# Performance work log

Hardware: AMD Instinct MI355X
Metric: run time of the kernel (lower is better)

The kernel has to match this reference:

```python
import jax, jax.numpy as jnp
import numpy as np

N = 50000        # num nodes (hyperedge ids also live in [0, N), matching old PyG quirk)
E = 1600000      # num incidence pairs
F_IN = 512       # input features
HEADS = 8
OUT1 = 8         # hconv1 out_channels per head
HID = HEADS * OUT1  # 64
NCLS = 7
NEG_SLOPE = 0.2


def setup_inputs() -> dict:
    key = jax.random.key(0)
    ks = jax.random.split(key, 8)
    x = jax.random.normal(ks[0], (N, F_IN), dtype=jnp.float32)
    edge_index = jax.random.randint(ks[1], (2, E), 0, N, dtype=jnp.int32)
    hyperedge_weight = jax.random.uniform(ks[2], (N,), dtype=jnp.float32) + 0.1
    W1 = jax.random.normal(ks[3], (F_IN, HEADS * OUT1), dtype=jnp.float32) * (1.0 / np.sqrt(F_IN))
    att1 = jax.random.normal(ks[4], (1, HEADS, 2 * OUT1), dtype=jnp.float32) * 0.1
    b1 = jnp.zeros((HEADS * OUT1,), dtype=jnp.float32)
    W2 = jax.random.normal(ks[5], (HID, NCLS), dtype=jnp.float32) * (1.0 / np.sqrt(HID))
    b2 = jnp.zeros((NCLS,), dtype=jnp.float32)
    return {"x": x, "edge_index": edge_index, "hyperedge_weight": hyperedge_weight,
            "W1": W1, "att1": att1, "b1": b1, "W2": W2, "b2": b2}


def _segment_softmax(a, seg, n):
    # numerically-stable softmax over groups defined by seg (per column / head)
    amax = jax.ops.segment_max(a, seg, num_segments=n)
    amax = jnp.where(jnp.isfinite(amax), amax, 0.0)
    ex = jnp.exp(a - amax[seg])
    den = jax.ops.segment_sum(ex, seg, num_segments=n)
    return ex / (den[seg] + 1e-16)


def _hconv(x, edge_index, hw, W, bias, heads, out_ch, att=None):
    """Old-PyG HypergraphConv forward (dropout disabled / eval mode)."""
    row, col = edge_index[0], edge_index[1]   # row: node ids, col: hyperedge ids
    n = x.shape[0]
    ones = jnp.ones(row.shape[0], dtype=x.dtype)
    xh = (x @ W).reshape(n, heads, out_ch)    # [N, H, C]

    if att is not None:
        # split att to avoid materializing cat([x_i, x_j]) per edge
        s_i = (xh * att[..., :out_ch]).sum(-1)   # [N, H]
        s_j = (xh * att[..., out_ch:]).sum(-1)   # [N, H]
        a = jax.nn.leaky_relu(s_i[row] + s_j[col], NEG_SLOPE)  # [E, H]
        alpha = _segment_softmax(a, row, n)      # grouped by source node
    else:
        alpha = None

    # node degree norm D (weighted by hyperedge weight)
    D = jax.ops.segment_sum(hw[col], row, num_segments=n)
    Dinv = jnp.where(D > 0, 1.0 / D, 0.0)
    # hyperedge degree norm B, scaled by hyperedge weight
    Bdeg = jax.ops.segment_sum(ones, col, num_segments=n)
    Binv = jnp.where(Bdeg > 0, 1.0 / Bdeg, 0.0) * hw

    # propagate 1: nodes -> hyperedges, norm = B[target]
    msg1 = xh[row] * Binv[col][:, None, None]          # [E, H, C]
    if alpha is not None:
        msg1 = msg1 * alpha[:, :, None]
    out_e = jax.ops.segment_sum(msg1, col, num_segments=n)  # [N, H, C]

    # propagate 2: hyperedges -> nodes, norm = D[target]
    msg2 = out_e[col] * Dinv[row][:, None, None]       # [E, H, C]
    if alpha is not None:
        msg2 = msg2 * alpha[:, :, None]
    out = jax.ops.segment_sum(msg2, row, num_segments=n)    # [N, H, C]

    return out.reshape(n, heads * out_ch) + bias   # concat=True


def reference(x, edge_index, hyperedge_weight, W1, att1, b1, W2, b2):
    # eval mode: F.dropout(p=0.6) is identity
    h = jax.nn.elu(_hconv(x, edge_index, hyperedge_weight, W1, b1, HEADS, OUT1, att1))
    out = _hconv(h, edge_index, hyperedge_weight, W2, b2, 1, NCLS, None)
    return jax.nn.log_softmax(out, axis=1)
```

## Files before the change

kernel.cpp:

```cpp
#include <hip/hip_runtime.h>
#include <hip/hip_bf16.h>
#include <cmath>

#define NN    50000
#define EE    1600000
#define FIN   512
#define NHEAD 8
#define OUT1  8
#define HID   64
#define NCLS  7

#define NB    391
#define EPB   4096
#define LOG2E 1.4426950408889634f

#define OFF_XH     0
#define OFF_SJ     3200000
#define OFF_SIRD   3600000
#define OFF_DINV   4400000
#define OFF_BINV   4450000
#define OFF_ACCE   4500000
#define OFF_H      7700000
#define OFF_XH2    10900000
#define OFF_ACCE2  11300000
#define OFF_RPTR   11700000
#define OFF_CPTR   11760000
#define OFF_BHR    11820000
#define OFF_BHC    11821000
#define OFF_BSR    11822000
#define OFF_BSC    11823000
#define OFF_BCR    11824000
#define OFF_BCC    11825000
#define OFF_CSRRC  11830000
#define OFF_CSRCR  13430000

#define LRELU(a) ((a) > 0.f ? (a) : 0.2f * (a))

__device__ __forceinline__ float fexp2(float x) {
#if __has_builtin(__builtin_amdgcn_exp2f)
  return __builtin_amdgcn_exp2f(x);
#else
  return exp2f(x);
#endif
}

__global__ __launch_bounds__(512) void zero_small(int* __restrict__ bh_r,
                                                  int* __restrict__ bh_c) {
  int t = threadIdx.x;
  if (t <= NB) { bh_r[t] = 0; bh_c[t] = 0; }
}

__global__ __launch_bounds__(256) void bucket_hist(const int* __restrict__ ei,
                                                   int* __restrict__ bh_r,
                                                   int* __restrict__ bh_c) {
  __shared__ int hr[NB], hc[NB];
  int t = threadIdx.x;
  for (int i = t; i < NB; i += 256) { hr[i] = 0; hc[i] = 0; }
  __syncthreads();
  for (int i = blockIdx.x * 256 + t; i < EE; i += gridDim.x * 256) {
    atomicAdd(hr + (ei[i] >> 7), 1);
    atomicAdd(hc + (ei[EE + i] >> 7), 1);
  }
  __syncthreads();
  for (int i = t; i < NB; i += 256) {
    if (hr[i]) atomicAdd(bh_r + i, hr[i]);
    if (hc[i]) atomicAdd(bh_c + i, hc[i]);
  }
}

__global__ __launch_bounds__(512) void bucket_scan(const int* __restrict__ bh_r,
                                                   const int* __restrict__ bh_c,
                                                   int* __restrict__ bs_r,
                                                   int* __restrict__ bs_c,
                                                   int* __restrict__ bc_r,
                                                   int* __restrict__ bc_c) {
  __shared__ int lds[512];
  int t = threadIdx.x;
  for (int side = 0; side < 2; ++side) {
    const int* bh = side ? bh_c : bh_r;
    int* bs = side ? bs_c : bs_r;
    int* bc = side ? bc_c : bc_r;
    int v = (t < NB) ? bh[t] : 0;
    lds[t] = v;
    __syncthreads();
    for (int off = 1; off < 512; off <<= 1) {
      int u = (t >= off) ? lds[t - off] : 0;
      __syncthreads();
      lds[t] += u;
      __syncthreads();
    }
    int excl = lds[t] - v;
    if (t <= NB) bs[t] = excl;
    if (t < NB) bc[t] = excl;
    __syncthreads();
  }
}

__global__ __launch_bounds__(256) void phaseA(const int* __restrict__ ei,
                                              int* __restrict__ bc_r,
                                              int* __restrict__ bc_c,
                                              int* __restrict__ tmp_r,
                                              int* __restrict__ tmp_c) {
  __shared__ int er[EPB];
  __shared__ int ec[EPB];
  __shared__ int hr[NB], hc[NB];
  const int e0 = blockIdx.x * EPB;
  const int cntE = min(EPB, EE - e0);
  const int t = threadIdx.x;
  for (int i = t; i < cntE; i += 256) { er[i] = ei[e0 + i]; ec[i] = ei[EE + e0 + i]; }
  for (int i = t; i < NB; i += 256) { hr[i] = 0; hc[i] = 0; }
  __syncthreads();
  for (int i = t; i < cntE; i += 256) {
    atomicAdd(hr + (er[i] >> 7), 1);
    atomicAdd(hc + (ec[i] >> 7), 1);
  }
  __syncthreads();
  for (int i = t; i < NB; i += 256) {
    int n = hr[i];
    hr[i] = n ? atomicAdd(bc_r + i, n) : 0;
    n = hc[i];
    hc[i] = n ? atomicAdd(bc_c + i, n) : 0;
  }
  __syncthreads();
  for (int i = t; i < cntE; i += 256) {
    int r = er[i], c = ec[i];
    int pr = atomicAdd(hr + (r >> 7), 1);
    tmp_r[pr] = ((r & 127) << 16) | c;
    int pc = atomicAdd(hc + (c >> 7), 1);
    tmp_c[pc] = ((c & 127) << 16) | r;
  }
}

__global__ __launch_bounds__(256) void phaseB(const int* __restrict__ tmp_r,
                                              const int* __restrict__ tmp_c,
                                              const int* __restrict__ bs_r,
                                              const int* __restrict__ bs_c,
                                              const float* __restrict__ hw,
                                              int* __restrict__ rptr,
                                              int* __restrict__ cptr,
                                              int* __restrict__ csr_row_c,
                                              int* __restrict__ csr_col_r,
                                              float* __restrict__ Binv) {
  const int side = blockIdx.x >= NB ? 1 : 0;
  const int b = blockIdx.x - side * NB;
  const int* tmp = side ? tmp_c : tmp_r;
  const int* bs = side ? bs_c : bs_r;
  int* ptr = side ? cptr : rptr;
  int* csr = side ? csr_col_r : csr_row_c;

  const int base = bs[b];
  const int M = bs[b + 1] - base;
  __shared__ int cnt[128], pre[128], cur[128];
  const int t = threadIdx.x;
  if (t < 128) cnt[t] = 0;
  __syncthreads();
  for (int i = t; i < M; i += 256) atomicAdd(cnt + (tmp[base + i] >> 16), 1);
  __syncthreads();
  if (t < 128) pre[t] = cnt[t];
  __syncthreads();
  for (int off = 1; off < 128; off <<= 1) {
    int u = (t >= off && t < 128) ? pre[t - off] : 0;
    __syncthreads();
    if (t < 128) pre[t] += u;
    __syncthreads();
  }
  const int node0 = b << 7;
  if (t < 128) {
    int excl = pre[t] - cnt[t];
    int g = node0 + t;
    if (g <= NN) ptr[g] = base + excl;
    cur[t] = base + excl;
    if (side && g < NN) Binv[g] = cnt[t] > 0 ? hw[g] / (float)cnt[t] : 0.f;
  }
  __syncthreads();
  for (int i = t; i < M; i += 256) {
    int e = tmp[base + i];
    int pos = atomicAdd(cur + (e >> 16), 1);
    csr[pos] = e & 0xFFFF;
  }
}

__global__ __launch_bounds__(256) void gemm1_kernel(const float* __restrict__ x,
                                                    const float* __restrict__ W1,
                                                    float* __restrict__ xh) {
  __shared__ float lx[32][68];
  __shared__ float lw[32][68];
  const int t = threadIdx.x;
  const int row0 = blockIdx.x * 64;
  const int ty = t >> 4, tx = t & 15;
  const int r0 = ty * 4, c0 = tx * 4;
  float acc[4][4] = {};

  for (int kb = 0; kb < FIN; kb += 32) {
    {
      int lr = t >> 2;
      int lk = (t & 3) * 8;
      int grow = row0 + lr;
      float4 a0, a1;
      if (grow < NN) {
        const float4* p = reinterpret_cast<const float4*>(x + (size_t)grow * FIN + kb + lk);
        a0 = p[0]; a1 = p[1];
      } else {
        a0 = make_float4(0.f, 0.f, 0.f, 0.f); a1 = a0;
      }
      lx[lk + 0][lr] = a0.x; lx[lk + 1][lr] = a0.y;
      lx[lk + 2][lr] = a0.z; lx[lk + 3][lr] = a0.w;
      lx[lk + 4][lr] = a1.x; lx[lk + 5][lr] = a1.y;
      lx[lk + 6][lr] = a1.z; lx[lk + 7][lr] = a1.w;
    }
    {
      int wk = t >> 3;
      int wc = (t & 7) * 8;
      const float4* q = reinterpret_cast<const float4*>(W1 + (size_t)(kb + wk) * HID + wc);
      float4 b0 = q[0], b1v = q[1];
      *reinterpret_cast<float4*>(&lw[wk][wc]) = b0;
      *reinterpret_cast<float4*>(&lw[wk][wc + 4]) = b1v;
    }
    __syncthreads();
#pragma unroll
    for (int kk = 0; kk < 32; ++kk) {
      const float4 af = *reinterpret_cast<const float4*>(&lx[kk][r0]);
      const float4 bf = *reinterpret_cast<const float4*>(&lw[kk][c0]);
      const float a4[4] = {af.x, af.y, af.z, af.w};
      const float b4[4] = {bf.x, bf.y, bf.z, bf.w};
#pragma unroll
      for (int i = 0; i < 4; ++i)
#pragma unroll
        for (int j = 0; j < 4; ++j)
          acc[i][j] = fmaf(a4[i], b4[j], acc[i][j]);
    }
    __syncthreads();
  }
#pragma unroll
  for (int i = 0; i < 4; ++i) {
    int gr = row0 + r0 + i;
    if (gr < NN) {
      float4 v = make_float4(acc[i][0], acc[i][1], acc[i][2], acc[i][3]);
      *reinterpret_cast<float4*>(xh + (size_t)gr * HID + c0) = v;
    }
  }
}

__global__ __launch_bounds__(256) void attscore_kernel(const float* __restrict__ xh,
                                                       const float* __restrict__ att1,
                                                       float2* __restrict__ sird,
                                                       float* __restrict__ s_j) {
  int t = blockIdx.x * 256 + threadIdx.x;
  if (t >= NN * NHEAD) return;
  int n = t >> 3, hh = t & 7;
  const float* xp = xh + (size_t)n * HID + hh * OUT1;
  float si = 0.f, sj = 0.f;
#pragma unroll
  for (int c = 0; c < OUT1; ++c) {
    float v = xp[c];
    si = fmaf(v, att1[hh * 16 + c], si);
    sj = fmaf(v, att1[hh * 16 + 8 + c], sj);
  }
  sird[t] = make_float2(si * LOG2E, 0.f);
  s_j[t] = sj * LOG2E;
}

__global__ __launch_bounds__(256) void den_csr(const int* __restrict__ rptr,
                                               const int* __restrict__ csr_row_c,
                                               const float* __restrict__ s_j,
                                               const float* __restrict__ hw,
                                               float2* __restrict__ sird,
                                               float* __restrict__ dinv) {
  int wid = (blockIdx.x * 256 + threadIdx.x) >> 6;
  int lane = threadIdx.x & 63;
  if (wid >= NN) return;
  int r = wid;
  int hh = lane & 7;
  int eslot = lane >> 3;
  float si = sird[r * 8 + hh].x;
  int beg = rptr[r], end = rptr[r + 1];
  float aexp = 0.f, ad = 0.f;
  int i = beg + eslot;
  for (; i + 8 < end; i += 16) {
    int c0 = csr_row_c[i], c1 = csr_row_c[i + 8];
    float sj0 = s_j[c0 * 8 + hh], sj1 = s_j[c1 * 8 + hh];
    float h0 = hw[c0], h1 = hw[c1];
    float a0 = LRELU(si + sj0), a1 = LRELU(si + sj1);
    aexp += fexp2(a0) + fexp2(a1);
    ad += h0 + h1;
  }
  if (i < end) {
    int c = csr_row_c[i];
    float a = LRELU(si + s_j[c * 8 + hh]);
    aexp += fexp2(a);
    ad += hw[c];
  }
  aexp += __shfl_xor(aexp, 8);
  aexp += __shfl_xor(aexp, 16);
  aexp += __shfl_xor(aexp, 32);
  ad += __shfl_xor(ad, 8);
  ad += __shfl_xor(ad, 16);
  ad += __shfl_xor(ad, 32);
  if (eslot == 0) {
    reinterpret_cast<float*>(sird)[(r * 8 + hh) * 2 + 1] = 1.0f / (aexp + 1e-16f);
    if (hh == 0) dinv[r] = ad > 0.f ? 1.0f / ad : 0.f;
  }
}

__global__ __launch_bounds__(256) void prop1_csr(const int* __restrict__ cptr,
                                                 const int* __restrict__ csr_col_r,
                                                 const float* __restrict__ xh,
                                                 const float2* __restrict__ sird,
                                                 const float* __restrict__ s_j,
                                                 const float* __restrict__ Binv,
                                                 float* __restrict__ acc_e) {
  int wid = (blockIdx.x * 256 + threadIdx.x) >> 6;
  int lane = threadIdx.x & 63;
  if (wid >= NN) return;
  const int c = wid;
  const int hh = lane >> 3;
  const int j = lane & 7;
  const int abase = lane & 56;
  float sj = s_j[c * 8 + hh];
  int beg = cptr[c], end = cptr[c + 1];
  float acc = 0.f;
  int i = beg;
  for (; i + 8 <= end; i += 8) {
    int rj = csr_col_r[i + j];
    float2 q = sird[rj * 8 + hh];
    float a = LRELU(q.x + sj);
    float aexp = fexp2(a) * q.y;
#pragma unroll
    for (int j2 = 0; j2 < 8; ++j2) {
      int r = __shfl(rj, j2);
      float al = __shfl(aexp, abase + j2);
      acc = fmaf(xh[(r << 6) + lane], al, acc);
    }
  }
  for (; i < end; ++i) {
    int r = csr_col_r[i];
    float2 q = sird[r * 8 + hh];
    float a = LRELU(q.x + sj);
    acc = fmaf(xh[(r << 6) + lane], fexp2(a) * q.y, acc);
  }
  acc_e[(c << 6) + lane] = acc * Binv[c];
}

__global__ __launch_bounds__(256) void prop2_csr(const int* __restrict__ rptr,
                                                 const int* __restrict__ csr_row_c,
                                                 const float* __restrict__ acc_e,
                                                 const float2* __restrict__ sird,
                                                 const float* __restrict__ s_j,
                                                 const float* __restrict__ dinv,
                                                 const float* __restrict__ b1,
                                                 float* __restrict__ h) {
  int wid = (blockIdx.x * 256 + threadIdx.x) >> 6;
  int lane = threadIdx.x & 63;
  if (wid >= NN) return;
  const int r = wid;
  const int hh = lane >> 3;
  const int j = lane & 7;
  const int abase = lane & 56;
  float2 sr = sird[r * 8 + hh];
  const float si = sr.x, rd = sr.y;
  int beg = rptr[r], end = rptr[r + 1];
  float acc = 0.f;
  int i = beg;
  for (; i + 8 <= end; i += 8) {
    int cj = csr_row_c[i + j];
    float sjv = s_j[cj * 8 + hh];
    float aexp = fexp2(LRELU(si + sjv));
#pragma unroll
    for (int j2 = 0; j2 < 8; ++j2) {
      int cc = __shfl(cj, j2);
      float al = __shfl(aexp, abase + j2);
      acc = fmaf(acc_e[(cc << 6) + lane], al, acc);
    }
  }
  for (; i < end; ++i) {
    int cc = csr_row_c[i];
    float aexp = fexp2(LRELU(si + s_j[cc * 8 + hh]));
    acc = fmaf(acc_e[(cc << 6) + lane], aexp, acc);
  }
  acc *= rd;
  float v = fmaf(acc, dinv[r], b1[lane]);
  h[(r << 6) + lane] = v > 0.f ? v : expm1f(v);
}

__global__ __launch_bounds__(256) void gemm2_kernel(const float* __restrict__ h,
                                                    const float* __restrict__ W2,
                                                    float* __restrict__ xh2) {
  int t = blockIdx.x * 256 + threadIdx.x;
  if (t >= NN * 8) return;
  int n = t >> 3, k = t & 7;
  if (k == 7) { xh2[t] = 0.f; return; }
  const float* hp = h + (size_t)n * HID;
  float acc = 0.f;
#pragma unroll
  for (int c = 0; c < HID; ++c) acc = fmaf(hp[c], W2[c * NCLS + k], acc);
  xh2[t] = acc;
}

__global__ __launch_bounds__(256) void prop3_csr(const int* __restrict__ cptr,
                                                 const int* __restrict__ csr_col_r,
                                                 const float* __restrict__ xh2,
                                                 const float* __restrict__ Binv,
                                                 float* __restrict__ acc_e2) {
  int t = blockIdx.x * 256 + threadIdx.x;
  int g = t >> 3, k = t & 7;
  if (g >= NN) return;
  int beg = cptr[g], end = cptr[g + 1];
  float acc = 0.f;
  int i = beg;
  for (; i + 3 < end; i += 4) {
    int r0 = csr_col_r[i], r1 = csr_col_r[i + 1];
    int r2 = csr_col_r[i + 2], r3 = csr_col_r[i + 3];
    float v0 = xh2[r0 * 8 + k], v1 = xh2[r1 * 8 + k];
    float v2 = xh2[r2 * 8 + k], v3 = xh2[r3 * 8 + k];
    acc += (v0 + v1) + (v2 + v3);
  }
  for (; i < end; ++i) acc += xh2[csr_col_r[i] * 8 + k];
  acc_e2[g * 8 + k] = acc * Binv[g];
}

__global__ __launch_bounds__(256) void prop4_csr(const int* __restrict__ rptr,
                                                 const int* __restrict__ csr_row_c,
                                                 const float* __restrict__ acc_e2,
                                                 const float* __restrict__ dinv,
                                                 const float* __restrict__ b2,
                                                 float* __restrict__ out) {
  int t = blockIdx.x * 256 + threadIdx.x;
  int r = t >> 3, k = t & 7;
  if (r >= NN) return;
  int beg = rptr[r], end = rptr[r + 1];
  float acc = 0.f;
  int i = beg;
  for (; i + 3 < end; i += 4) {
    int c0 = csr_row_c[i], c1 = csr_row_c[i + 1];
    int c2 = csr_row_c[i + 2], c3 = csr_row_c[i + 3];
    float v0 = acc_e2[c0 * 8 + k], v1 = acc_e2[c1 * 8 + k];
    float v2 = acc_e2[c2 * 8 + k], v3 = acc_e2[c3 * 8 + k];
    acc += (v0 + v1) + (v2 + v3);
  }
  for (; i < end; ++i) acc += acc_e2[csr_row_c[i] * 8 + k];
  float v = (k < NCLS) ? fmaf(acc, dinv[r], b2[k]) : -INFINITY;
  float m = v;
  m = fmaxf(m, __shfl_xor(m, 1, 8));
  m = fmaxf(m, __shfl_xor(m, 2, 8));
  m = fmaxf(m, __shfl_xor(m, 4, 8));
  float ex = (k < NCLS) ? expf(v - m) : 0.f;
  float s = ex;
  s += __shfl_xor(s, 1, 8);
  s += __shfl_xor(s, 2, 8);
  s += __shfl_xor(s, 4, 8);
  float lse = m + logf(s);
  if (k < NCLS) out[(size_t)r * NCLS + k] = v - lse;
}

extern "C" void kernel_launch(void* const* d_in, const int* in_sizes, int n_in,
                              void* d_out, int out_size, void* d_ws, size_t ws_size,
                              hipStream_t stream) {
  const float* x    = (const float*)d_in[0];
  const int*   ei   = (const int*)d_in[1];
  const float* hw   = (const float*)d_in[2];
  const float* W1   = (const float*)d_in[3];
  const float* att1 = (const float*)d_in[4];
  const float* b1   = (const float*)d_in[5];
  const float* W2   = (const float*)d_in[6];
  const float* b2   = (const float*)d_in[7];
  float* out = (float*)d_out;
  float* ws  = (float*)d_ws;

  float* xh     = ws + OFF_XH;
  float* s_j    = ws + OFF_SJ;
  float2* sird  = (float2*)(ws + OFF_SIRD);
  float* dinv   = ws + OFF_DINV;
  float* Binv   = ws + OFF_BINV;
  float* acc_e  = ws + OFF_ACCE;
  float* hbuf   = ws + OFF_H;
  float* xh2    = ws + OFF_XH2;
  float* acc_e2 = ws + OFF_ACCE2;
  int* rptr = (int*)(ws + OFF_RPTR);
  int* cptr = (int*)(ws + OFF_CPTR);
  int* bh_r = (int*)(ws + OFF_BHR);
  int* bh_c = (int*)(ws + OFF_BHC);
  int* bs_r = (int*)(ws + OFF_BSR);
  int* bs_c = (int*)(ws + OFF_BSC);
  int* bc_r = (int*)(ws + OFF_BCR);
  int* bc_c = (int*)(ws + OFF_BCC);
  int* csr_row_c = (int*)(ws + OFF_CSRRC);
  int* csr_col_r = (int*)(ws + OFF_CSRCR);
  int* tmp_r = (int*)(ws + OFF_XH);
  int* tmp_c = (int*)(ws + OFF_ACCE);

  zero_small<<<1, 512, 0, stream>>>(bh_r, bh_c);
  bucket_hist<<<256, 256, 0, stream>>>(ei, bh_r, bh_c);
  bucket_scan<<<1, 512, 0, stream>>>(bh_r, bh_c, bs_r, bs_c, bc_r, bc_c);
  phaseA<<<(EE + EPB - 1) / EPB, 256, 0, stream>>>(ei, bc_r, bc_c, tmp_r, tmp_c);
  phaseB<<<2 * NB, 256, 0, stream>>>(tmp_r, tmp_c, bs_r, bs_c, hw,
                                     rptr, cptr, csr_row_c, csr_col_r, Binv);

  gemm1_kernel<<<(NN + 63) / 64, 256, 0, stream>>>(x, W1, xh);
  attscore_kernel<<<(NN * NHEAD + 255) / 256, 256, 0, stream>>>(xh, att1, sird, s_j);
  den_csr<<<(NN * 64 + 255) / 256, 256, 0, stream>>>(rptr, csr_row_c, s_j, hw, sird, dinv);
  prop1_csr<<<(NN * 64 + 255) / 256, 256, 0, stream>>>(cptr, csr_col_r, xh, sird, s_j, Binv, acc_e);
  prop2_csr<<<(NN * 64 + 255) / 256, 256, 0, stream>>>(rptr, csr_row_c, acc_e, sird, s_j,
                                                       dinv, b1, hbuf);

  gemm2_kernel<<<(NN * 8 + 255) / 256, 256, 0, stream>>>(hbuf, W2, xh2);
  prop3_csr<<<(NN * 8 + 255) / 256, 256, 0, stream>>>(cptr, csr_col_r, xh2, Binv, acc_e2);
  prop4_csr<<<(NN * 8 + 255) / 256, 256, 0, stream>>>(rptr, csr_row_c, acc_e2, dinv, b2, out);
}
```

Before: 354.0 us.

## Double-buffer LDS tiles in gemm1 with register prefetch of next K-slice

```diff
diff --git a/kernel.cpp b/kernel.cpp
--- a/kernel.cpp
+++ b/kernel.cpp
@@ -183,44 +183,66 @@
 __global__ __launch_bounds__(256) void gemm1_kernel(const float* __restrict__ x,
                                                     const float* __restrict__ W1,
                                                     float* __restrict__ xh) {
-  __shared__ float lx[32][68];
-  __shared__ float lw[32][68];
+  __shared__ float lx[2][32][68];
+  __shared__ float lw[2][32][68];
   const int t = threadIdx.x;
   const int row0 = blockIdx.x * 64;
   const int ty = t >> 4, tx = t & 15;
   const int r0 = ty * 4, c0 = tx * 4;
+  const bool isX = t < 128;
+  const int srow = t & 63;
+  const int sk = (t >> 6) * 16;
+  const int wu = t - 128;
+  const int wk = wu >> 2;
+  const int wc = (wu & 3) * 16;
+
+  float4 p0, p1, p2, p3;
+
+#define G1_PREFETCH(kb)                                                      \
+  {                                                                          \
+    if (isX) {                                                               \
+      int grow = row0 + srow;                                                \
+      if (grow < NN) {                                                       \
+        const float4* p = reinterpret_cast<const float4*>(                   \
+            x + (size_t)grow * FIN + (kb) + sk);                             \
+        p0 = p[0]; p1 = p[1]; p2 = p[2]; p3 = p[3];                          \
+      } else {                                                               \
+        p0 = make_float4(0.f, 0.f, 0.f, 0.f); p1 = p0; p2 = p0; p3 = p0;     \
+      }                                                                      \
+    } else {                                                                 \
+      const float4* q = reinterpret_cast<const float4*>(                     \
+          W1 + (size_t)((kb) + wk) * HID + wc);                              \
+      p0 = q[0]; p1 = q[1]; p2 = q[2]; p3 = q[3];                            \
+    }                                                                        \
+  }
+
+#define G1_COMMIT(buf)                                                       \
+  {                                                                          \
+    if (isX) {                                                               \
+      float v[16] = {p0.x, p0.y, p0.z, p0.w, p1.x, p1.y, p1.z, p1.w,         \
+                     p2.x, p2.y, p2.z, p2.w, p3.x, p3.y, p3.z, p3.w};        \
+      _Pragma("unroll")                                                      \
+      for (int i = 0; i < 16; ++i) lx[buf][sk + i][srow] = v[i];             \
+    } else {                                                                 \
+      *reinterpret_cast<float4*>(&lw[buf][wk][wc + 0])  = p0;                \
+      *reinterpret_cast<float4*>(&lw[buf][wk][wc + 4])  = p1;                \
+      *reinterpret_cast<float4*>(&lw[buf][wk][wc + 8])  = p2;                \
+      *reinterpret_cast<float4*>(&lw[buf][wk][wc + 12]) = p3;                \
+    }                                                                        \
+  }
+
   float acc[4][4] = {};
-
-  for (int kb = 0; kb < FIN; kb += 32) {
-    {
-      int lr = t >> 2;
-      int lk = (t & 3) * 8;
-      int grow = row0 + lr;
-      float4 a0, a1;
-      if (grow < NN) {
-        const float4* p = reinterpret_cast<const float4*>(x + (size_t)grow * FIN + kb + lk);
-        a0 = p[0]; a1 = p[1];
-      } else {
-        a0 = make_float4(0.f, 0.f, 0.f, 0.f); a1 = a0;
-      }
-      lx[lk + 0][lr] = a0.x; lx[lk + 1][lr] = a0.y;
-      lx[lk + 2][lr] = a0.z; lx[lk + 3][lr] = a0.w;
-      lx[lk + 4][lr] = a1.x; lx[lk + 5][lr] = a1.y;
-      lx[lk + 6][lr] = a1.z; lx[lk + 7][lr] = a1.w;
-    }
-    {
-      int wk = t >> 3;
-      int wc = (t & 7) * 8;
-      const float4* q = reinterpret_cast<const float4*>(W1 + (size_t)(kb + wk) * HID + wc);
-      float4 b0 = q[0], b1v = q[1];
-      *reinterpret_cast<float4*>(&lw[wk][wc]) = b0;
-      *reinterpret_cast<float4*>(&lw[wk][wc + 4]) = b1v;
-    }
-    __syncthreads();
+  G1_PREFETCH(0);
+  G1_COMMIT(0);
+  __syncthreads();
+
+  for (int tt = 0; tt < FIN / 32; ++tt) {
+    const int cur = tt & 1;
+    if (tt < FIN / 32 - 1) G1_PREFETCH((tt + 1) * 32);
 #pragma unroll
     for (int kk = 0; kk < 32; ++kk) {
-      const float4 af = *reinterpret_cast<const float4*>(&lx[kk][r0]);
-      const float4 bf = *reinterpret_cast<const float4*>(&lw[kk][c0]);
+      const float4 af = *reinterpret_cast<const float4*>(&lx[cur][kk][r0]);
+      const float4 bf = *reinterpret_cast<const float4*>(&lw[cur][kk][c0]);
       const float a4[4] = {af.x, af.y, af.z, af.w};
       const float b4[4] = {bf.x, bf.y, bf.z, bf.w};
 #pragma unroll
@@ -229,8 +251,12 @@
         for (int j = 0; j < 4; ++j)
           acc[i][j] = fmaf(a4[i], b4[j], acc[i][j]);
     }
+    if (tt < FIN / 32 - 1) G1_COMMIT(cur ^ 1);
     __syncthreads();
   }
+#undef G1_PREFETCH
+#undef G1_COMMIT
+
 #pragma unroll
   for (int i = 0; i < 4; ++i) {
     int gr = row0 + r0 + i;
```

Result: slower. 383.7 us (+8.4%).

## Split gemm1 K dimension across two blocks and reduce partials in attscore

Applied to the files above, without the earlier changes.

```diff
diff --git a/kernel.cpp b/kernel.cpp
--- a/kernel.cpp
+++ b/kernel.cpp
@@ -182,35 +182,37 @@
 
 __global__ __launch_bounds__(256) void gemm1_kernel(const float* __restrict__ x,
                                                     const float* __restrict__ W1,
-                                                    float* __restrict__ xh) {
-  __shared__ float lx[32][68];
+                                                    float* __restrict__ p0,
+                                                    float* __restrict__ p1) {
+  __shared__ float lx[32][66];
   __shared__ float lw[32][68];
   const int t = threadIdx.x;
   const int row0 = blockIdx.x * 64;
+  const int kbase = blockIdx.y * (FIN / 2);
+  float* __restrict__ dst = blockIdx.y ? p1 : p0;
   const int ty = t >> 4, tx = t & 15;
   const int r0 = ty * 4, c0 = tx * 4;
+  const int sr = t >> 2;
+  const int sk = (t & 3) * 8;
+  const int grow = row0 + sr;
+  const int wk = t >> 3;
+  const int wc = (t & 7) * 8;
+
   float acc[4][4] = {};
 
-  for (int kb = 0; kb < FIN; kb += 32) {
+  for (int kb = kbase; kb < kbase + FIN / 2; kb += 32) {
     {
-      int lr = t >> 2;
-      int lk = (t & 3) * 8;
-      int grow = row0 + lr;
-      float4 a0, a1;
+      float4 a0 = make_float4(0.f, 0.f, 0.f, 0.f), a1 = a0;
       if (grow < NN) {
-        const float4* p = reinterpret_cast<const float4*>(x + (size_t)grow * FIN + kb + lk);
+        const float4* p = reinterpret_cast<const float4*>(x + (size_t)grow * FIN + kb + sk);
         a0 = p[0]; a1 = p[1];
-      } else {
-        a0 = make_float4(0.f, 0.f, 0.f, 0.f); a1 = a0;
       }
-      lx[lk + 0][lr] = a0.x; lx[lk + 1][lr] = a0.y;
-      lx[lk + 2][lr] = a0.z; lx[lk + 3][lr] = a0.w;
-      lx[lk + 4][lr] = a1.x; lx[lk + 5][lr] = a1.y;
-      lx[lk + 6][lr] = a1.z; lx[lk + 7][lr] = a1.w;
+      lx[sk + 0][sr] = a0.x; lx[sk + 1][sr] = a0.y;
+      lx[sk + 2][sr] = a0.z; lx[sk + 3][sr] = a0.w;
+      lx[sk + 4][sr] = a1.x; lx[sk + 5][sr] = a1.y;
+      lx[sk + 6][sr] = a1.z; lx[sk + 7][sr] = a1.w;
     }
     {
-      int wk = t >> 3;
-      int wc = (t & 7) * 8;
       const float4* q = reinterpret_cast<const float4*>(W1 + (size_t)(kb + wk) * HID + wc);
       float4 b0 = q[0], b1v = q[1];
       *reinterpret_cast<float4*>(&lw[wk][wc]) = b0;
@@ -236,26 +238,34 @@
     int gr = row0 + r0 + i;
     if (gr < NN) {
       float4 v = make_float4(acc[i][0], acc[i][1], acc[i][2], acc[i][3]);
-      *reinterpret_cast<float4*>(xh + (size_t)gr * HID + c0) = v;
-    }
-  }
-}
-
-__global__ __launch_bounds__(256) void attscore_kernel(const float* __restrict__ xh,
+      *reinterpret_cast<float4*>(dst + (size_t)gr * HID + c0) = v;
+    }
+  }
+}
+
+__global__ __launch_bounds__(256) void attscore_kernel(float* __restrict__ xh,
+                                                       const float* __restrict__ p1,
                                                        const float* __restrict__ att1,
                                                        float2* __restrict__ sird,
                                                        float* __restrict__ s_j) {
   int t = blockIdx.x * 256 + threadIdx.x;
   if (t >= NN * NHEAD) return;
-  int n = t >> 3, hh = t & 7;
-  const float* xp = xh + (size_t)n * HID + hh * OUT1;
+  int hh = t & 7;
+  const size_t base = (size_t)t * 8;
+  float4 a0 = *reinterpret_cast<const float4*>(xh + base);
+  float4 a1 = *reinterpret_cast<const float4*>(xh + base + 4);
+  float4 q0 = *reinterpret_cast<const float4*>(p1 + base);
+  float4 q1 = *reinterpret_cast<const float4*>(p1 + base + 4);
+  float v[8] = {a0.x + q0.x, a0.y + q0.y, a0.z + q0.z, a0.w + q0.w,
+                a1.x + q1.x, a1.y + q1.y, a1.z + q1.z, a1.w + q1.w};
   float si = 0.f, sj = 0.f;
 #pragma unroll
   for (int c = 0; c < OUT1; ++c) {
-    float v = xp[c];
-    si = fmaf(v, att1[hh * 16 + c], si);
-    sj = fmaf(v, att1[hh * 16 + 8 + c], sj);
-  }
+    si = fmaf(v[c], att1[hh * 16 + c], si);
+    sj = fmaf(v[c], att1[hh * 16 + 8 + c], sj);
+  }
+  *reinterpret_cast<float4*>(xh + base)     = make_float4(v[0], v[1], v[2], v[3]);
+  *reinterpret_cast<float4*>(xh + base + 4) = make_float4(v[4], v[5], v[6], v[7]);
   sird[t] = make_float2(si * LOG2E, 0.f);
   s_j[t] = sj * LOG2E;
 }
@@ -495,8 +505,11 @@
   phaseB<<<2 * NB, 256, 0, stream>>>(tmp_r, tmp_c, bs_r, bs_c, hw,
                                      rptr, cptr, csr_row_c, csr_col_r, Binv);
 
-  gemm1_kernel<<<(NN + 63) / 64, 256, 0, stream>>>(x, W1, xh);
-  attscore_kernel<<<(NN * NHEAD + 255) / 256, 256, 0, stream>>>(xh, att1, sird, s_j);
+  {
+    dim3 g((NN + 63) / 64, 2);
+    gemm1_kernel<<<g, 256, 0, stream>>>(x, W1, xh, hbuf);
+  }
+  attscore_kernel<<<(NN * NHEAD + 255) / 256, 256, 0, stream>>>(xh, hbuf, att1, sird, s_j);
   den_csr<<<(NN * 64 + 255) / 256, 256, 0, stream>>>(rptr, csr_row_c, s_j, hw, sird, dinv);
   prop1_csr<<<(NN * 64 + 255) / 256, 256, 0, stream>>>(cptr, csr_col_r, xh, sird, s_j, Binv, acc_e);
   prop2_csr<<<(NN * 64 + 255) / 256, 256, 0, stream>>>(rptr, csr_row_c, acc_e, sird, s_j,
```

New measurement: 348.5 us. No clear change (-1.5%).
